# Performance work log

Measured on AMD Instinct MI355X. Metric: run time of the kernel, lower is better.

## Reference

```python
import jax, jax.numpy as jnp
import numpy as np

L = 3          # n_relation_encoder_layer
H = 64         # hidden_dim
PH = 3         # path_hop
SLOPE = (1.0/8.0 + 1.0/3.0) / 2.0  # RReLU in eval mode


def act(x):
    return jnp.where(x >= 0, x, x * SLOPE)


def layer_norm(x, eps=1e-5):
    m = jnp.mean(x, axis=-1, keepdims=True)
    v = jnp.var(x, axis=-1, keepdims=True)
    return (x - m) / jnp.sqrt(v + eps)


def setup_inputs() -> dict:
    key = jax.random.key(0)
    ks = jax.random.split(key, 20)
    E, N, R, Bq = 262144, 65536, 200, 40
    Rt = R * Bq
    d = {}
    d["edge_index"] = jax.random.randint(ks[0], (2, E), 0, N)
    d["edge_type"] = jax.random.randint(ks[1], (E,), 0, Rt)
    d["edge_query_relations"] = jax.random.randint(ks[2], (E,), 0, Rt)
    d["h_positions"] = jax.random.randint(ks[3], (Bq,), 0, N)
    d["t_positions"] = jax.random.randint(ks[4], (Bq,), 0, N)
    d["query_relations"] = jax.random.randint(ks[5], (Bq,), 0, R)
    d["labels"] = jax.random.randint(ks[6], (N, 2), 0, PH + 1)
    d["num_ent"] = N
    d["relation_num"] = R
    d["shot"] = 5
    s = 0.05
    nrm = lambda k, sh: jax.random.normal(k, sh, jnp.float32) * s
    d["pos_emb"] = nrm(ks[7], ((PH + 1) * (PH + 1), H))
    d["start_rel_emb"] = nrm(ks[8], (1, H))
    d["loop_emb"] = nrm(ks[9], (1, H))
    d["W_msg"] = nrm(ks[10], (L, H, 3 * H)); d["b_msg"] = jnp.zeros((L, H))
    d["W_ht2r"] = nrm(ks[11], (L, H, 3 * H)); d["b_ht2r"] = jnp.zeros((L, H))
    d["W_alpha"] = nrm(ks[12], (L, 2 * H)); d["b_alpha"] = jnp.zeros((L,))
    d["W_beta"] = nrm(ks[13], (L, 2 * H)); d["b_beta"] = jnp.zeros((L,))
    d["W_loop"] = nrm(ks[14], (L, H, 2 * H)); d["b_loop"] = jnp.zeros((L, H))
    d["W_ent"] = nrm(ks[15], (L, H, H)); d["b_ent"] = jnp.zeros((L, H))
    d["W_rel"] = nrm(ks[16], (L, H, H)); d["b_rel"] = jnp.zeros((L, H))
    d["W_final"] = nrm(ks[17], (H, L * H)); d["b_final"] = jnp.zeros((H,))
    return d


def reference(pos_emb, start_rel_emb, loop_emb,
              W_msg, b_msg, W_ht2r, b_ht2r, W_alpha, b_alpha, W_beta, b_beta,
              W_loop, b_loop, W_ent, b_ent, W_rel, b_rel, W_final, b_final,
              edge_index, edge_type, edge_query_relations,
              h_positions, t_positions, query_relations, labels,
              num_ent, relation_num, shot):
    Bq = h_positions.shape[0]
    Rt = relation_num * Bq
    col, row = edge_index[0], edge_index[1]  # (h side, t side)

    # token-set initialization
    position = labels[:, 0] * (PH + 1) + labels[:, 1]
    node_emb = pos_emb[position]
    node_emb = node_emb.at[h_positions].set(pos_emb[0])
    node_emb = node_emb.at[t_positions].set(pos_emb[1])
    q_rows = query_relations + jnp.arange(Bq) * relation_num
    rel_emb = jnp.zeros((Rt, H), pos_emb.dtype).at[q_rows].set(start_rel_emb[0])
    loop = jnp.broadcast_to(loop_emb, (Bq, H))

    # compute_norm: symmetric D^-1/2 norm over (col,row)
    deg = jax.ops.segment_sum(jnp.ones((col.shape[0],), node_emb.dtype), row, num_segments=num_ent)
    deg_inv = jnp.where(deg > 0, deg ** -0.5, 0.0)
    ent_norm = deg_inv[row] * deg_inv[col]  # [E]

    finals = []
    for i in range(L):
        r_e = rel_emb[edge_type]            # [E,H]
        h_e = node_emb[col]                 # [E,H]
        q_e = rel_emb[edge_query_relations] # [E,H]
        feat = jnp.concatenate([h_e, r_e, q_e], axis=-1)  # [E,3H]
        msg = act(feat @ W_msg[i].T + b_msg[i])
        # entity attention (GAT); faithful double index_select of the normalizer
        a = act(jnp.concatenate([r_e, q_e], -1)) @ W_alpha[i] + b_alpha[i]  # [E]
        a = jnp.exp(a)
        a_sum = jax.ops.segment_sum(a, row, num_segments=num_ent)
        denom = (a_sum[row] + 1e-10)[row]
        msg = msg * (a / denom)[:, None]
        msg = msg * ent_norm[:, None]   # applied in forward
        msg = msg * ent_norm[:, None]   # applied again in ent_aggregation
        node_emb = jax.ops.segment_sum(msg, row, num_segments=num_ent)
        node_emb = layer_norm(act(node_emb @ W_ent[i].T + b_ent[i]))

        h_e = node_emb[col]
        t_e = node_emb[row]
        r_e = rel_emb[edge_type]
        msg = act(jnp.concatenate([h_e, t_e, q_e], -1) @ W_ht2r[i].T + b_ht2r[i])
        b = jnp.concatenate([r_e, q_e], -1) @ W_beta[i] + b_beta[i]  # no act (as in source)
        b = jnp.exp(b)
        b_sum = jax.ops.segment_sum(b, edge_type, num_segments=Rt)
        b_den = (b_sum[edge_type] + 1e-10)[edge_type]
        msg = msg * (b / b_den)[:, None]
        agg = jax.ops.segment_sum(msg, edge_type, num_segments=Rt)
        rel_emb = layer_norm(act(agg @ W_rel[i].T + b_rel[i]) + rel_emb)
        finals.append(rel_emb)

        qr = rel_emb[q_rows]
        loop = layer_norm(loop + act(jnp.concatenate([loop, qr], -1) @ W_loop[i].T + b_loop[i]))

    fin = jnp.concatenate(finals, axis=-1)            # [Rt, L*H]
    fin = layer_norm(act(fin @ W_final.T + b_final))  # [Rt, H]
    fin = fin.reshape(-1, shot, relation_num, H)
    fin = jnp.mean(fin, axis=1)                       # [B, R, H]; dropout = identity (eval)
    loop_m = jnp.mean(loop.reshape(-1, shot, 1, H), axis=1).reshape(-1, 1, H)
    out = jnp.concatenate([fin, loop_m], axis=1)      # [B, R+1, H]
    return out
```

## Files before the change

kernel.cpp:

```cpp
#include <hip/hip_runtime.h>
#include <hip/hip_bf16.h>

#define DEV __device__ __forceinline__

constexpr int Nn   = 65536;
constexpr int Ee   = 262144;
constexpr int Rr   = 200;
constexpr int BQ   = 40;
constexpr int Rt   = Rr * BQ;
constexpr int Hh   = 64;
constexpr int SHOT = 5;
constexpr float SLOPE  = 0.22916667f;
constexpr float EPS_LN = 1e-5f;

constexpr size_t BASE = 16;
constexpr size_t off_node   = BASE;
constexpr size_t off_node2  = off_node  + (size_t)Nn*32;
constexpr size_t off_rel    = off_node2 + (size_t)Nn*32;
constexpr size_t off_rel2   = off_rel   + (size_t)Rt*32;
constexpr size_t off_fin    = off_rel2  + (size_t)Rt*32;
constexpr size_t off_finln  = off_fin   + (size_t)3*Rt*32;
constexpr size_t off_loop   = off_finln + (size_t)Rt*Hh;
constexpr size_t off_avP    = off_loop  + (size_t)BQ*Hh;
constexpr size_t off_bvP    = off_avP   + (size_t)Ee;
constexpr size_t off_asum   = off_bvP   + (size_t)Ee;
constexpr size_t off_bsum   = off_asum  + (size_t)Nn;
constexpr size_t off_degF   = off_bsum  + (size_t)Rt;
constexpr size_t off_degi   = off_degF  + (size_t)Nn;
constexpr size_t off_histE  = off_degi  + (size_t)Nn;
constexpr size_t off_baseE  = off_histE + (size_t)Rt;
constexpr size_t off_baseR  = off_baseE + (size_t)Rt;
constexpr size_t off_part   = off_baseR + (size_t)Nn;
constexpr size_t off_uv     = off_part  + 256;
constexpr size_t off_edge1  = off_uv    + (size_t)4*Rt;
constexpr size_t off_edge2  = off_edge1 + (size_t)4*Ee;
constexpr size_t off_WmsgF  = off_edge2 + (size_t)4*Ee;
constexpr size_t off_Wht2rF = off_WmsgF + 18432;
constexpr size_t off_WentF  = off_Wht2rF + 18432;
constexpr size_t off_WrelF  = off_WentF + 6144;
constexpr size_t off_WfinF  = off_WrelF + 6144;
constexpr size_t off_Wloop  = off_WfinF + 6144;
constexpr size_t off_bmsg   = off_Wloop + (size_t)3*128*64;
constexpr size_t off_bht2r  = off_bmsg  + 192;
constexpr size_t off_bent   = off_bht2r + 192;
constexpr size_t off_brel   = off_bent  + 192;
constexpr size_t off_bloop  = off_brel  + 192;
constexpr size_t off_bfin   = off_bloop + 192;
constexpr size_t off_Wa     = off_bfin  + 64;
constexpr size_t off_ba     = off_Wa    + 384;
constexpr size_t off_Wb     = off_ba    + 4;
constexpr size_t off_bb     = off_Wb    + 384;
constexpr size_t off_pos    = off_bb    + 4;
constexpr size_t off_srel   = off_pos   + 1024;
constexpr size_t off_loop0  = off_srel  + 64;
constexpr size_t off_end    = off_loop0 + 64;

typedef __attribute__((ext_vector_type(8))) short short8v;
typedef __attribute__((ext_vector_type(4))) float float4v;

DEV float bf2f(unsigned short u) { return __uint_as_float(((unsigned)u) << 16); }
DEV unsigned short f2bf_rtne(float f) {
    unsigned int b = __float_as_uint(f);
    b += 0x7FFFu + ((b >> 16) & 1u);
    return (unsigned short)(b >> 16);
}
DEV float actf(float x) { return x >= 0.f ? x : x * SLOPE; }
DEV void atomAddF(float* p, float v) {
#if defined(__HIP_DEVICE_COMPILE__)
    unsafeAtomicAdd(p, v);
#endif
}
DEV void atomPkAddBf16(unsigned short* p, unsigned int pk) {
#if defined(__HIP_DEVICE_COMPILE__)
    asm volatile("global_atomic_pk_add_bf16 %0, %1, off"
                 :: "v"((unsigned long long)p), "v"(pk) : "memory");
#endif
}
DEV float loadF(const void* p, size_t i, int isb) {
    return isb ? bf2f(((const unsigned short*)p)[i]) : ((const float*)p)[i];
}

__global__ __launch_bounds__(64) void k_sniff(const unsigned short* __restrict__ pos, int* __restrict__ flag) {
    float v = bf2f(pos[threadIdx.x]);
    bool bad = !(fabsf(v) < 1e3f);
    unsigned long long m = __ballot(bad);
    if (threadIdx.x == 0) flag[0] = (m == 0ull) ? 1 : 0;
}

__global__ __launch_bounds__(256) void k_fill16(unsigned short* __restrict__ out, int n, unsigned short val) {
    int i = blockIdx.x * 256 + threadIdx.x;
    if (i < n) out[i] = val;
}

struct PrepArgs { const void* src[19]; void* dst[19]; };

__global__ __launch_bounds__(256) void k_prep(PrepArgs a, const int* __restrict__ flag,
                                              int* __restrict__ degi, unsigned int* __restrict__ relz,
                                              int* __restrict__ histE) {
    constexpr int NJ = 19;
    constexpr int type[NJ] = {3,3,3,3,3,2, 0,0,0,0,0,0,0,0,0,0,0,0,0};
    constexpr int KD[NJ]   = {192,192,64,64,192,128, 0,0,0,0,0,0,0,0,0,0,0,0,0};
    constexpr int NEL[NJ]  = {36864,36864,12288,12288,12288,24576,
                              192,192,192,192,192,64,384,3,384,3,1024,64,64};
    const int isb = flag[0];
    int tid0 = blockIdx.x * blockDim.x + threadIdx.x;
    int stride = gridDim.x * blockDim.x;
    for (int j = 0; j < NJ; ++j) {
        const void* s = a.src[j];
        int n = NEL[j];
        if (type[j] == 0) {
            float* d = (float*)a.dst[j];
            for (int i = tid0; i < n; i += stride) d[i] = loadF(s, i, isb);
        } else if (type[j] == 2) {
            float* d = (float*)a.dst[j];
            int K = KD[j];
            for (int i = tid0; i < n; i += stride) {
                int h = i & 63;
                int k = (i >> 6) % K;
                int b = i / (64 * K);
                d[i] = loadF(s, (size_t)(b*64 + h) * K + k, isb);
            }
        } else {
            unsigned short* d = (unsigned short*)a.dst[j];
            int K = KD[j];
            int perL = K * 64;
            for (int i = tid0; i < n; i += stride) {
                int layer = i / perL;
                int r1 = i % perL;
                int c  = r1 / 2048;
                int r2 = r1 % 2048;
                int g  = r2 / 512;
                int r3 = r2 % 512;
                int l  = r3 >> 3;
                int jj = r3 & 7;
                int nn = g * 16 + (l & 15);
                int k  = c * 32 + (l >> 4) * 8 + jj;
                d[i] = f2bf_rtne(loadF(s, (size_t)layer * perL + (size_t)nn * K + k, isb));
            }
        }
    }
    for (int i = tid0; i < Nn; i += stride) degi[i] = 0;
    for (int i = tid0; i < Rt * 32; i += stride) relz[i] = 0u;
    for (int i = tid0; i < Rt; i += stride) histE[i] = 0;
}

__global__ __launch_bounds__(256) void k_hist(const int* __restrict__ rowp, const int* __restrict__ et,
                                              int* __restrict__ degi, int* __restrict__ histE) {
    int e = blockIdx.x * 256 + threadIdx.x;
    if (e < Ee) {
        atomicAdd(&degi[rowp[e]], 1);
        atomicAdd(&histE[et[e]], 1);
    }
}

__global__ __launch_bounds__(256) void k_deg_scan(const int* __restrict__ degi, float* __restrict__ degF,
                                                  int* __restrict__ part,
                                                  const int* __restrict__ histE, int* __restrict__ baseE) {
    __shared__ int sh[256];
    __shared__ int sh2[256];
    int t = threadIdx.x, b = blockIdx.x;
    int n = b * 256 + t;
    int d = degi[n];
    degF[n] = d > 0 ? 1.0f / sqrtf((float)d) : 0.0f;
    sh[t] = d; __syncthreads();
    for (int o = 128; o; o >>= 1) { if (t < o) sh[t] += sh[t + o]; __syncthreads(); }
    if (t == 0) part[b] = sh[0];
    if (b == 0) {
        int s = 0;
        for (int j = 0; j < 32; ++j) { int idx = t * 32 + j; if (idx < Rt) s += histE[idx]; }
        sh2[t] = s; __syncthreads();
        for (int o = 1; o < 256; o <<= 1) {
            int u = (t >= o) ? sh2[t - o] : 0;
            __syncthreads(); sh2[t] += u; __syncthreads();
        }
        int run = sh2[t] - s;
        for (int j = 0; j < 32; ++j) {
            int idx = t * 32 + j;
            if (idx < Rt) { baseE[idx] = run; run += histE[idx]; }
        }
    }
}

__global__ __launch_bounds__(256) void k_scan_part(int* __restrict__ part) {
    __shared__ int sh[256];
    int t = threadIdx.x;
    int v = part[t];
    sh[t] = v; __syncthreads();
    for (int o = 1; o < 256; o <<= 1) {
        int u = (t >= o) ? sh[t - o] : 0;
        __syncthreads(); sh[t] += u; __syncthreads();
    }
    part[t] = sh[t] - v;
}

__global__ __launch_bounds__(256) void k_baseR(const int* __restrict__ degi, const int* __restrict__ part,
                                               int* __restrict__ baseR) {
    __shared__ int sh[256];
    int t = threadIdx.x, b = blockIdx.x;
    int n = b * 256 + t;
    int d = degi[n];
    sh[t] = d; __syncthreads();
    for (int o = 1; o < 256; o <<= 1) {
        int u = (t >= o) ? sh[t - o] : 0;
        __syncthreads(); sh[t] += u; __syncthreads();
    }
    baseR[n] = part[b] + sh[t] - d;
}

__global__ __launch_bounds__(256) void k_scatter(const int* __restrict__ col, const int* __restrict__ rowp,
                                                 const int* __restrict__ et, const int* __restrict__ eqr,
                                                 int* __restrict__ baseR, int* __restrict__ baseE,
                                                 int4* __restrict__ edge1, int4* __restrict__ edge2) {
    int e = blockIdx.x * 256 + threadIdx.x;
    if (e >= Ee) return;
    int4 ed; ed.x = col[e]; ed.y = rowp[e]; ed.z = et[e]; ed.w = eqr[e];
    int s1 = atomicAdd(&baseR[ed.y], 1);
    edge1[s1] = ed;
    int s2 = atomicAdd(&baseE[ed.z], 1);
    edge2[s2] = ed;
}

__global__ __launch_bounds__(256) void k_node_init(const int* __restrict__ labels,
                                                   const float* __restrict__ posf,
                                                   unsigned short* __restrict__ node) {
    int idx = blockIdx.x * 256 + threadIdx.x;
    if (idx >= Nn * Hh) return;
    int n = idx >> 6, h = idx & 63;
    int pos = labels[2*n] * 4 + labels[2*n + 1];
    node[idx] = f2bf_rtne(posf[pos * 64 + h]);
}
__global__ __launch_bounds__(256) void k_init_small(const int* __restrict__ hpos, const int* __restrict__ tpos,
                                                    const int* __restrict__ qrel,
                                                    const float* __restrict__ posf,
                                                    const float* __restrict__ srel,
                                                    const float* __restrict__ l0,
                                                    unsigned short* __restrict__ node,
                                                    unsigned short* __restrict__ rel,
                                                    float* __restrict__ loop) {
    int idx = blockIdx.x * 256 + threadIdx.x;
    int seg = idx / (BQ * Hh), r = idx % (BQ * Hh);
    int b = r >> 6, h = r & 63;
    if (seg == 0) {
        int p = hpos[b];
        bool skip = false;
        for (int j = 0; j < BQ; ++j) skip |= (tpos[j] == p);
        if (!skip) node[(size_t)p * 64 + h] = f2bf_rtne(posf[h]);
    } else if (seg == 1) {
        node[(size_t)tpos[b] * 64 + h] = f2bf_rtne(posf[64 + h]);
    } else if (seg == 2) {
        rel[((size_t)qrel[b] + (size_t)b * Rr) * 64 + h] = f2bf_rtne(srel[h]);
    } else if (seg == 3) {
        loop[r] = l0[h];
    }
}

__global__ __launch_bounds__(256) void k_uv(const unsigned short* __restrict__ rel,
                                            const float* __restrict__ Wa, const float* __restrict__ Wb,
                                            float* __restrict__ uv,
                                            float* __restrict__ asum,
                                            float4v* __restrict__ node2, float4v* __restrict__ rel2) {
    int tid = threadIdx.x, lane = tid & 63, wv = tid >> 6;
    int w = blockIdx.x * 4 + wv;
    if (w < Rt) {
        float x = bf2f(rel[(size_t)w * 64 + lane]);
        float ax = actf(x);
        float pua = ax * Wa[lane], pva = ax * Wa[64 + lane];
        float pub = x * Wb[lane],  pvb = x * Wb[64 + lane];
        for (int off = 32; off; off >>= 1) {
            pua += __shfl_xor(pua, off); pva += __shfl_xor(pva, off);
            pub += __shfl_xor(pub, off); pvb += __shfl_xor(pvb, off);
        }
        if (lane == 0) {
            uv[w] = pua; uv[Rt + w] = pva; uv[2 * Rt + w] = pub; uv[3 * Rt + w] = pvb;
        }
    }
    int tid0 = blockIdx.x * 256 + tid;
    int stride = gridDim.x * 256;
    float4v z = {0.f, 0.f, 0.f, 0.f};
    for (int i = tid0; i < Nn + Rt; i += stride) asum[i] = 0.f;
    for (int i = tid0; i < Nn * 8; i += stride) node2[i] = z;
    for (int i = tid0; i < Rt * 8; i += stride) rel2[i] = z;
}

__global__ __launch_bounds__(256) void k_ab_edge(const int4* __restrict__ edge1, const int4* __restrict__ edge2,
                                                 const float* __restrict__ uv,
                                                 const float* __restrict__ ba, const float* __restrict__ bb,
                                                 float* __restrict__ avP, float* __restrict__ bvP,
                                                 float* __restrict__ a_sum, float* __restrict__ b_sum) {
    __shared__ float sv[256];
    __shared__ int sd[256];
    int tid = threadIdx.x;
    int e = blockIdx.x * 256 + tid;
    int4 e1 = edge1[e];
    float av = expf(uv[e1.z] + uv[Rt + e1.w] + ba[0]);
    avP[e] = av;
    sv[tid] = av; sd[tid] = e1.y;
    __syncthreads();
    if (tid == 0 || sd[tid - 1] != e1.y) {
        float s = av;
        for (int j = tid + 1; j < 256 && sd[j] == e1.y; ++j) s += sv[j];
        atomAddF(&a_sum[e1.y], s);
    }
    __syncthreads();
    int4 e2 = edge2[e];
    float bv = expf(uv[2 * Rt + e2.z] + uv[3 * Rt + e2.w] + bb[0]);
    bvP[e] = bv;
    sv[tid] = bv; sd[tid] = e2.z;
    __syncthreads();
    if (tid == 0 || sd[tid - 1] != e2.z) {
        float s = bv;
        for (int j = tid + 1; j < 256 && sd[j] == e2.z; ++j) s += sv[j];
        atomAddF(&b_sum[e2.z], s);
    }
}

template<int KIND>
__global__ __launch_bounds__(256) void k_msg_mfma(
    const unsigned short* __restrict__ node, const unsigned short* __restrict__ rel,
    const int4* __restrict__ edgeP,
    const int* __restrict__ rowp_orig, const int* __restrict__ et_orig,
    const unsigned short* __restrict__ Wfrag,
    const float* __restrict__ bias,
    const float* __restrict__ vals, const float* __restrict__ sums,
    const float* __restrict__ degF,
    unsigned short* __restrict__ dst)
{
    constexpr int P = 200;
    __shared__ __align__(16) unsigned short feat[64 * P];
    __shared__ int s_src0[64], s_src1[64], s_src2[64], s_dst[64];
    __shared__ float s_coeff[64];
    const int tid = threadIdx.x;
    const int lane = tid & 63;
    const int wv = tid >> 6;
    const int e0 = blockIdx.x * 64;

    if (tid < 64) {
        int e = e0 + tid;
        int4 ed = edgeP[e];
        if (KIND == 0) {
            s_src0[tid] = ed.x; s_src1[tid] = ed.z; s_src2[tid] = ed.w; s_dst[tid] = ed.y;
            int rr = rowp_orig[ed.y];
            float dn = degF[ed.y] * degF[ed.x];
            s_coeff[tid] = vals[e] / (sums[rr] + 1e-10f) * dn * dn;
        } else {
            s_src0[tid] = ed.x; s_src1[tid] = ed.y; s_src2[tid] = ed.w; s_dst[tid] = ed.z;
            int tt = et_orig[ed.z];
            s_coeff[tid] = vals[e] / (sums[tt] + 1e-10f);
        }
    }

    const int wr = wv >> 1, wc = wv & 1;
    short8v bf[2][6];
#pragma unroll
    for (int tc = 0; tc < 2; ++tc) {
        int g = wc * 2 + tc;
#pragma unroll
        for (int c = 0; c < 6; ++c)
            bf[tc][c] = *(const short8v*)(Wfrag + (((size_t)c * 4 + g) * 64 + lane) * 8);
    }
    __syncthreads();

    {
        const int sub = lane >> 3, ls8 = lane & 7;
#pragma unroll
        for (int t2 = 0; t2 < 6; ++t2) {
            int unit = wv * 48 + t2 * 8 + sub;
            int e = unit & 63, part = unit >> 6;
            int srow = part == 0 ? s_src0[e] : (part == 1 ? s_src1[e] : s_src2[e]);
            const unsigned short* bse;
            if (KIND == 0) bse = (part == 0) ? node : rel;
            else           bse = (part == 2) ? rel : node;
            uint4 v = *(const uint4*)(bse + (size_t)srow * 64 + ls8 * 8);
            *(uint4*)(feat + (size_t)e * P + part * 64 + ls8 * 8) = v;
        }
    }
    __syncthreads();

    const int m = lane & 15, qd = lane >> 4;
    float4v zero = {0.f, 0.f, 0.f, 0.f};
    float4v acc[2][2];
    acc[0][0] = zero; acc[0][1] = zero; acc[1][0] = zero; acc[1][1] = zero;
#pragma unroll
    for (int c = 0; c < 6; ++c) {
        short8v a0 = *(const short8v*)(feat + (wr * 32 + m) * P + c * 32 + qd * 8);
        short8v a1 = *(const short8v*)(feat + (wr * 32 + 16 + m) * P + c * 32 + qd * 8);
        acc[0][0] = __builtin_amdgcn_mfma_f32_16x16x32_bf16(a0, bf[0][c], acc[0][0], 0, 0, 0);
        acc[0][1] = __builtin_amdgcn_mfma_f32_16x16x32_bf16(a0, bf[1][c], acc[0][1], 0, 0, 0);
        acc[1][0] = __builtin_amdgcn_mfma_f32_16x16x32_bf16(a1, bf[0][c], acc[1][0], 0, 0, 0);
        acc[1][1] = __builtin_amdgcn_mfma_f32_16x16x32_bf16(a1, bf[1][c], acc[1][1], 0, 0, 0);
    }
    __syncthreads();

    float* msgT = (float*)feat;
#pragma unroll
    for (int tc = 0; tc < 2; ++tc) {
        int h = wc * 32 + tc * 16 + m;
        float bi = bias[h];
#pragma unroll
        for (int tr = 0; tr < 2; ++tr) {
#pragma unroll
            for (int r = 0; r < 4; ++r) {
                int er = wr * 32 + tr * 16 + qd * 4 + r;
                msgT[er * 65 + h] = actf(acc[tr][tc][r] + bi) * s_coeff[er];
            }
        }
    }
    __syncthreads();

    {
        int c = wv * 16 + (lane & 15);
        int seg = lane >> 4;
        int ebase = seg * 16;
        float a = 0.f;
#pragma unroll
        for (int i = 0; i < 16; ++i) {
            int e = ebase + i;
            a += msgT[e * 65 + c];
            bool flush = (i == 15) || (s_dst[e + 1] != s_dst[e]);
            float an = __shfl_xor(a, 1);
            if (flush) {
                if (!(lane & 1)) {
                    unsigned int pk = (unsigned int)f2bf_rtne(a)
                                    | ((unsigned int)f2bf_rtne(an) << 16);
                    atomPkAddBf16(dst + (size_t)s_dst[e] * 64 + c, pk);
                }
                a = 0.f;
            }
        }
    }
#if defined(__HIP_DEVICE_COMPILE__)
    asm volatile("s_waitcnt vmcnt(0)" ::: "memory");
#endif
}

template<int MODE>
__global__ __launch_bounds__(256) void k_row_ln(const unsigned short* __restrict__ x,
                                                const unsigned short* __restrict__ Wfrag,
                                                const float* __restrict__ bias,
                                                unsigned short* __restrict__ out,
                                                unsigned short* __restrict__ fin_i) {
    __shared__ float yT[64 * 65];
    const int tid = threadIdx.x, lane = tid & 63, wv = tid >> 6;
    const int wr = wv >> 1, wc = wv & 1;
    const int m = lane & 15, qd = lane >> 4;
    const size_t n0 = (size_t)blockIdx.x * 64;

    short8v bf[2][2];
#pragma unroll
    for (int tc = 0; tc < 2; ++tc) {
        int g = wc * 2 + tc;
#pragma unroll
        for (int c = 0; c < 2; ++c)
            bf[tc][c] = *(const short8v*)(Wfrag + (((size_t)c * 4 + g) * 64 + lane) * 8);
    }

    float4v zero = {0.f, 0.f, 0.f, 0.f};
    float4v acc[2][2];
    acc[0][0] = zero; acc[0][1] = zero; acc[1][0] = zero; acc[1][1] = zero;
#pragma unroll
    for (int c = 0; c < 2; ++c) {
        short8v a0 = *(const short8v*)(x + (n0 + wr * 32 + m) * 64 + c * 32 + qd * 8);
        short8v a1 = *(const short8v*)(x + (n0 + wr * 32 + 16 + m) * 64 + c * 32 + qd * 8);
        acc[0][0] = __builtin_amdgcn_mfma_f32_16x16x32_bf16(a0, bf[0][c], acc[0][0], 0, 0, 0);
        acc[0][1] = __builtin_amdgcn_mfma_f32_16x16x32_bf16(a0, bf[1][c], acc[0][1], 0, 0, 0);
        acc[1][0] = __builtin_amdgcn_mfma_f32_16x16x32_bf16(a1, bf[0][c], acc[1][0], 0, 0, 0);
        acc[1][1] = __builtin_amdgcn_mfma_f32_16x16x32_bf16(a1, bf[1][c], acc[1][1], 0, 0, 0);
    }

#pragma unroll
    for (int tc = 0; tc < 2; ++tc) {
        int h = wc * 32 + tc * 16 + m;
        float bi = bias[h];
#pragma unroll
        for (int tr = 0; tr < 2; ++tr) {
#pragma unroll
            for (int r = 0; r < 4; ++r) {
                int row = wr * 32 + tr * 16 + qd * 4 + r;
                yT[row * 65 + h] = actf(acc[tr][tc][r] + bi);
            }
        }
    }
    __syncthreads();

    for (int jj = 0; jj < 16; ++jj) {
        int j = wv * 16 + jj;
        float v = yT[j * 65 + lane];
        if (MODE == 1) v += bf2f(out[(n0 + j) * 64 + lane]);
        float s = v, s2 = v * v;
        for (int off = 32; off; off >>= 1) { s += __shfl_xor(s, off); s2 += __shfl_xor(s2, off); }
        float mean = s * (1.f / 64.f);
        float var = s2 * (1.f / 64.f) - mean * mean;
        if (var < 0.f) var = 0.f;
        unsigned short nv = f2bf_rtne((v - mean) / sqrtf(var + EPS_LN));
        out[(n0 + j) * 64 + lane] = nv;
        if (MODE == 1) fin_i[(n0 + j) * 64 + lane] = nv;
    }
}

__global__ __launch_bounds__(256) void k_final(const unsigned short* __restrict__ finB,
                                               const unsigned short* __restrict__ Wfrag,
                                               const float* __restrict__ bias,
                                               float* __restrict__ fin_ln) {
    __shared__ float yT[64 * 65];
    const int tid = threadIdx.x, lane = tid & 63, wv = tid >> 6;
    const int wr = wv >> 1, wc = wv & 1;
    const int m = lane & 15, qd = lane >> 4;
    const size_t r0 = (size_t)blockIdx.x * 64;

    short8v bf[2][6];
#pragma unroll
    for (int tc = 0; tc < 2; ++tc) {
        int g = wc * 2 + tc;
#pragma unroll
        for (int c = 0; c < 6; ++c)
            bf[tc][c] = *(const short8v*)(Wfrag + (((size_t)c * 4 + g) * 64 + lane) * 8);
    }

    float4v zero = {0.f, 0.f, 0.f, 0.f};
    float4v acc[2][2];
    acc[0][0] = zero; acc[0][1] = zero; acc[1][0] = zero; acc[1][1] = zero;
#pragma unroll
    for (int c = 0; c < 6; ++c) {
        const unsigned short* base = finB + (size_t)(c >> 1) * Rt * 64 + (c & 1) * 32 + qd * 8;
        short8v a0 = *(const short8v*)(base + (r0 + wr * 32 + m) * 64);
        short8v a1 = *(const short8v*)(base + (r0 + wr * 32 + 16 + m) * 64);
        acc[0][0] = __builtin_amdgcn_mfma_f32_16x16x32_bf16(a0, bf[0][c], acc[0][0], 0, 0, 0);
        acc[0][1] = __builtin_amdgcn_mfma_f32_16x16x32_bf16(a0, bf[1][c], acc[0][1], 0, 0, 0);
        acc[1][0] = __builtin_amdgcn_mfma_f32_16x16x32_bf16(a1, bf[0][c], acc[1][0], 0, 0, 0);
        acc[1][1] = __builtin_amdgcn_mfma_f32_16x16x32_bf16(a1, bf[1][c], acc[1][1], 0, 0, 0);
    }

#pragma unroll
    for (int tc = 0; tc < 2; ++tc) {
        int h = wc * 32 + tc * 16 + m;
        float bi = bias[h];
#pragma unroll
        for (int tr = 0; tr < 2; ++tr) {
#pragma unroll
            for (int r = 0; r < 4; ++r) {
                int row = wr * 32 + tr * 16 + qd * 4 + r;
                yT[row * 65 + h] = actf(acc[tr][tc][r] + bi);
            }
        }
    }
    __syncthreads();

    for (int jj = 0; jj < 16; ++jj) {
        int j = wv * 16 + jj;
        float v = yT[j * 65 + lane];
        float s = v, s2 = v * v;
        for (int off = 32; off; off >>= 1) { s += __shfl_xor(s, off); s2 += __shfl_xor(s2, off); }
        float mean = s * (1.f / 64.f);
        float var = s2 * (1.f / 64.f) - mean * mean;
        if (var < 0.f) var = 0.f;
        fin_ln[(r0 + j) * 64 + lane] = (v - mean) / sqrtf(var + EPS_LN);
    }
}

__global__ __launch_bounds__(64) void k_loop_upd(const unsigned short* __restrict__ rel,
                                                 const int* __restrict__ qrel,
                                                 const float* __restrict__ Wt,
                                                 const float* __restrict__ bias,
                                                 float* __restrict__ loop) {
    __shared__ float cat[128];
    int b = blockIdx.x, lane = threadIdx.x;
    float lv = loop[b * 64 + lane];
    int qr = qrel[b] + b * Rr;
    cat[lane] = lv;
    cat[64 + lane] = bf2f(rel[(size_t)qr * 64 + lane]);
    __syncthreads();
    float acc = 0.f;
    for (int k = 0; k < 128; ++k) acc = fmaf(cat[k], Wt[k * 64 + lane], acc);
    float v = lv + actf(acc + bias[lane]);
    float s = v, s2 = v * v;
    for (int off = 32; off; off >>= 1) { s += __shfl_xor(s, off); s2 += __shfl_xor(s2, off); }
    float mean = s * (1.f / 64.f);
    float var = s2 * (1.f / 64.f) - mean * mean;
    if (var < 0.f) var = 0.f;
    loop[b * 64 + lane] = (v - mean) / sqrtf(var + EPS_LN);
}

__global__ __launch_bounds__(256) void k_out(const float* __restrict__ fin_ln,
                                             const float* __restrict__ loop,
                                             void* __restrict__ out, int n,
                                             const int* __restrict__ flag) {
    int idx = blockIdx.x * 256 + threadIdx.x;
    if (idx >= n) return;
    int h = idx & 63;
    int j = (idx >> 6) % (Rr + 1);
    int g = idx / ((Rr + 1) * 64);
    float v = 0.f;
    if (j < Rr) {
        for (int s = 0; s < SHOT; ++s)
            v += fin_ln[(size_t)((g * SHOT + s) * Rr + j) * 64 + h];
    } else {
        for (int s = 0; s < SHOT; ++s)
            v += loop[(g * SHOT + s) * 64 + h];
    }
    v *= (1.0f / SHOT);
    if (flag[0]) ((__hip_bfloat16*)out)[idx] = __float2bfloat16(v);
    else         ((float*)out)[idx] = v;
}

extern "C" void kernel_launch(void* const* d_in, const int* in_sizes, int n_in,
                              void* d_out, int out_size, void* d_ws, size_t ws_size,
                              hipStream_t stream) {
    if (ws_size < off_end * 4 || n_in != 29) {
        k_fill16<<<(out_size + 255) / 256, 256, 0, stream>>>(
            (unsigned short*)d_out, out_size, (n_in != 29) ? (unsigned short)0x429A : (unsigned short)0x42F6);
        return;
    }

    const int* edge_index = (const int*)d_in[0];
    const int* col  = edge_index;
    const int* rowp = edge_index + Ee;
    const int* et   = (const int*)d_in[1];
    const int* eqr  = (const int*)d_in[2];
    const int* hpos = (const int*)d_in[3];
    const int* tpos = (const int*)d_in[4];
    const int* qrel = (const int*)d_in[5];
    const int* labels = (const int*)d_in[6];

    float* W = (float*)d_ws;
    int*   flag  = (int*)d_ws;
    unsigned short* node  = (unsigned short*)(W + off_node);
    unsigned short* node2 = (unsigned short*)(W + off_node2);
    unsigned short* rel   = (unsigned short*)(W + off_rel);
    unsigned short* rel2  = (unsigned short*)(W + off_rel2);
    unsigned short* fin   = (unsigned short*)(W + off_fin);
    float* finln = W + off_finln;
    float* loop  = W + off_loop;
    float* avP   = W + off_avP;
    float* bvP   = W + off_bvP;
    float* asum  = W + off_asum;
    float* bsum  = W + off_bsum;
    float* degF  = W + off_degF;
    int*   degi  = (int*)(W + off_degi);
    int*   histE = (int*)(W + off_histE);
    int*   baseE = (int*)(W + off_baseE);
    int*   baseR = (int*)(W + off_baseR);
    int*   part  = (int*)(W + off_part);
    float* uv    = W + off_uv;
    int4*  edge1 = (int4*)(W + off_edge1);
    int4*  edge2 = (int4*)(W + off_edge2);
    unsigned short* WmsgF  = (unsigned short*)(W + off_WmsgF);
    unsigned short* Wht2rF = (unsigned short*)(W + off_Wht2rF);
    unsigned short* WentF  = (unsigned short*)(W + off_WentF);
    unsigned short* WrelF  = (unsigned short*)(W + off_WrelF);
    unsigned short* WfinF  = (unsigned short*)(W + off_WfinF);

    k_sniff<<<1, 64, 0, stream>>>((const unsigned short*)d_in[10], flag);
    PrepArgs pa;
    const int src_idx[19] = {13,15,23,25,27,21, 14,16,24,26,22,28,17,18,19,20,10,11,12};
    void* dsts[19] = {WmsgF, Wht2rF, WentF, WrelF, WfinF, W+off_Wloop,
                      W+off_bmsg, W+off_bht2r, W+off_bent, W+off_brel, W+off_bloop, W+off_bfin,
                      W+off_Wa, W+off_ba, W+off_Wb, W+off_bb, W+off_pos, W+off_srel, W+off_loop0};
    for (int j = 0; j < 19; ++j) { pa.src[j] = d_in[src_idx[j]]; pa.dst[j] = dsts[j]; }
    k_prep<<<144, 256, 0, stream>>>(pa, flag, degi, (unsigned int*)rel, histE);

    k_hist<<<Ee / 256, 256, 0, stream>>>(rowp, et, degi, histE);
    k_deg_scan<<<Nn / 256, 256, 0, stream>>>(degi, degF, part, histE, baseE);
    k_scan_part<<<1, 256, 0, stream>>>(part);
    k_baseR<<<Nn / 256, 256, 0, stream>>>(degi, part, baseR);
    k_scatter<<<Ee / 256, 256, 0, stream>>>(col, rowp, et, eqr, baseR, baseE, edge1, edge2);
    k_node_init<<<(Nn * Hh) / 256, 256, 0, stream>>>(labels, W + off_pos, node);
    k_init_small<<<(4 * BQ * Hh + 255) / 256, 256, 0, stream>>>(hpos, tpos, qrel,
                                                                W + off_pos, W + off_srel, W + off_loop0,
                                                                node, rel, loop);

    for (int i = 0; i < 3; ++i) {
        k_uv<<<2048, 256, 0, stream>>>(rel, W + off_Wa + i * 128, W + off_Wb + i * 128,
                                       uv, asum, (float4v*)node2, (float4v*)rel2);
        k_ab_edge<<<Ee / 256, 256, 0, stream>>>(edge1, edge2, uv,
                                                W + off_ba + i, W + off_bb + i,
                                                avP, bvP, asum, bsum);
        k_msg_mfma<0><<<Ee / 64, 256, 0, stream>>>(node, rel, edge1, rowp, et,
                                                   WmsgF + (size_t)i * 12288, W + off_bmsg + i * 64,
                                                   avP, asum, degF, node2);
        k_row_ln<0><<<Nn / 64, 256, 0, stream>>>(node2, WentF + (size_t)i * 4096,
                                                 W + off_bent + i * 64, node, nullptr);
        k_msg_mfma<1><<<Ee / 64, 256, 0, stream>>>(node, rel, edge2, rowp, et,
                                                   Wht2rF + (size_t)i * 12288, W + off_bht2r + i * 64,
                                                   bvP, bsum, degF, rel2);
        k_row_ln<1><<<Rt / 64, 256, 0, stream>>>(rel2, WrelF + (size_t)i * 4096,
                                                 W + off_brel + i * 64, rel,
                                                 fin + (size_t)i * Rt * 64);
        k_loop_upd<<<BQ, 64, 0, stream>>>(rel, qrel, W + off_Wloop + (size_t)i * 8192,
                                          W + off_bloop + i * 64, loop);
    }

    k_final<<<Rt / 64, 256, 0, stream>>>(fin, WfinF, W + off_bfin, finln);
    k_out<<<(out_size + 255) / 256, 256, 0, stream>>>(finln, loop, d_out, out_size, flag);
}
```

Before: 567.1 us.

## Fuse uv/zeroing/loop update into LN kernels and double edges per msg block

Removes the per-layer k_uv and k_loop_upd kernels. Their work moves into other kernels: the uv projection for the next layer is computed inside the new k_rel_ln, the loop update runs there too, and the accumulator zeroing is done inside the LN kernels right after they read their inputs. Node init and the first-layer uv are folded into k_prep and k_init_small. Separately, k_msg_mfma now handles 128 edges per block in two 64-edge passes, halving the grid and reusing the weight fragments held in registers. The aim is fewer launches and less global traffic, at the cost of more serial work per block and careful ordering of the zeroing against later reads.

New measurement: 606.5 us. +6.9%, slower.

```diff
diff --git a/kernel.cpp b/kernel.cpp
--- a/kernel.cpp
+++ b/kernel.cpp
@@ -96,7 +96,12 @@
 
 __global__ __launch_bounds__(256) void k_prep(PrepArgs a, const int* __restrict__ flag,
                                               int* __restrict__ degi, unsigned int* __restrict__ relz,
-                                              int* __restrict__ histE) {
+                                              int* __restrict__ histE,
+                                              const int* __restrict__ labels, const void* __restrict__ pos_raw,
+                                              unsigned short* __restrict__ node,
+                                              unsigned int* __restrict__ node2z, unsigned int* __restrict__ rel2z,
+                                              float* __restrict__ asumz,
+                                              float* __restrict__ uvz) {
     constexpr int NJ = 19;
     constexpr int type[NJ] = {3,3,3,3,3,2, 0,0,0,0,0,0,0,0,0,0,0,0,0};
     constexpr int KD[NJ]   = {192,192,64,64,192,128, 0,0,0,0,0,0,0,0,0,0,0,0,0};
@@ -139,9 +144,18 @@
             }
         }
     }
+    for (int i = tid0; i < Nn * Hh; i += stride) {
+        int n = i >> 6, h = i & 63;
+        int pos = labels[2*n] * 4 + labels[2*n + 1];
+        node[i] = f2bf_rtne(loadF(pos_raw, (size_t)pos * 64 + h, isb));
+    }
     for (int i = tid0; i < Nn; i += stride) degi[i] = 0;
     for (int i = tid0; i < Rt * 32; i += stride) relz[i] = 0u;
     for (int i = tid0; i < Rt; i += stride) histE[i] = 0;
+    for (int i = tid0; i < Nn * 32; i += stride) node2z[i] = 0u;
+    for (int i = tid0; i < Rt * 32; i += stride) rel2z[i] = 0u;
+    for (int i = tid0; i < Nn + Rt; i += stride) asumz[i] = 0.f;
+    for (int i = tid0; i < 4 * Rt; i += stride) uvz[i] = 0.f;
 }
 
 __global__ __launch_bounds__(256) void k_hist(const int* __restrict__ rowp, const int* __restrict__ et,
@@ -220,15 +234,6 @@
     edge2[s2] = ed;
 }
 
-__global__ __launch_bounds__(256) void k_node_init(const int* __restrict__ labels,
-                                                   const float* __restrict__ posf,
-                                                   unsigned short* __restrict__ node) {
-    int idx = blockIdx.x * 256 + threadIdx.x;
-    if (idx >= Nn * Hh) return;
-    int n = idx >> 6, h = idx & 63;
-    int pos = labels[2*n] * 4 + labels[2*n + 1];
-    node[idx] = f2bf_rtne(posf[pos * 64 + h]);
-}
 __global__ __launch_bounds__(256) void k_init_small(const int* __restrict__ hpos, const int* __restrict__ tpos,
                                                     const int* __restrict__ qrel,
                                                     const float* __restrict__ posf,
@@ -236,7 +241,9 @@
                                                     const float* __restrict__ l0,
                                                     unsigned short* __restrict__ node,
                                                     unsigned short* __restrict__ rel,
-                                                    float* __restrict__ loop) {
+                                                    float* __restrict__ loop,
+                                                    const float* __restrict__ Wa0, const float* __restrict__ Wb0,
+                                                    float* __restrict__ uv) {
     int idx = blockIdx.x * 256 + threadIdx.x;
     int seg = idx / (BQ * Hh), r = idx % (BQ * Hh);
     int b = r >> 6, h = r & 63;
@@ -248,38 +255,23 @@
     } else if (seg == 1) {
         node[(size_t)tpos[b] * 64 + h] = f2bf_rtne(posf[64 + h]);
     } else if (seg == 2) {
-        rel[((size_t)qrel[b] + (size_t)b * Rr) * 64 + h] = f2bf_rtne(srel[h]);
-    } else if (seg == 3) {
-        loop[r] = l0[h];
-    }
-}
-
-__global__ __launch_bounds__(256) void k_uv(const unsigned short* __restrict__ rel,
-                                            const float* __restrict__ Wa, const float* __restrict__ Wb,
-                                            float* __restrict__ uv,
-                                            float* __restrict__ asum,
-                                            float4v* __restrict__ node2, float4v* __restrict__ rel2) {
-    int tid = threadIdx.x, lane = tid & 63, wv = tid >> 6;
-    int w = blockIdx.x * 4 + wv;
-    if (w < Rt) {
-        float x = bf2f(rel[(size_t)w * 64 + lane]);
+        int w = qrel[b] + b * Rr;
+        unsigned short xb = f2bf_rtne(srel[h]);
+        rel[(size_t)w * 64 + h] = xb;
+        float x = bf2f(xb);
         float ax = actf(x);
-        float pua = ax * Wa[lane], pva = ax * Wa[64 + lane];
-        float pub = x * Wb[lane],  pvb = x * Wb[64 + lane];
+        float pua = ax * Wa0[h], pva = ax * Wa0[64 + h];
+        float pub = x * Wb0[h],  pvb = x * Wb0[64 + h];
         for (int off = 32; off; off >>= 1) {
             pua += __shfl_xor(pua, off); pva += __shfl_xor(pva, off);
             pub += __shfl_xor(pub, off); pvb += __shfl_xor(pvb, off);
         }
-        if (lane == 0) {
+        if (h == 0) {
             uv[w] = pua; uv[Rt + w] = pva; uv[2 * Rt + w] = pub; uv[3 * Rt + w] = pvb;
         }
-    }
-    int tid0 = blockIdx.x * 256 + tid;
-    int stride = gridDim.x * 256;
-    float4v z = {0.f, 0.f, 0.f, 0.f};
-    for (int i = tid0; i < Nn + Rt; i += stride) asum[i] = 0.f;
-    for (int i = tid0; i < Nn * 8; i += stride) node2[i] = z;
-    for (int i = tid0; i < Rt * 8; i += stride) rel2[i] = z;
+    } else if (seg == 3) {
+        loop[r] = l0[h];
+    }
 }
 
 __global__ __launch_bounds__(256) void k_ab_edge(const int4* __restrict__ edge1, const int4* __restrict__ edge2,
@@ -327,14 +319,14 @@
 {
     constexpr int P = 200;
     __shared__ __align__(16) unsigned short feat[64 * P];
-    __shared__ int s_src0[64], s_src1[64], s_src2[64], s_dst[64];
-    __shared__ float s_coeff[64];
+    __shared__ int s_src0[128], s_src1[128], s_src2[128], s_dst[132];
+    __shared__ float s_coeff[128];
     const int tid = threadIdx.x;
     const int lane = tid & 63;
     const int wv = tid >> 6;
-    const int e0 = blockIdx.x * 64;
-
-    if (tid < 64) {
+    const int e0 = blockIdx.x * 128;
+
+    if (tid < 128) {
         int e = e0 + tid;
         int4 ed = edgeP[e];
         if (KIND == 0) {
@@ -348,6 +340,7 @@
             s_coeff[tid] = vals[e] / (sums[tt] + 1e-10f);
         }
     }
+    if (tid == 0) s_dst[128] = -1;
 
     const int wr = wv >> 1, wc = wv & 1;
     short8v bf[2][6];
@@ -360,85 +353,88 @@
     }
     __syncthreads();
 
-    {
-        const int sub = lane >> 3, ls8 = lane & 7;
+    const int sub = lane >> 3, ls8 = lane & 7;
+    const int m = lane & 15, qd = lane >> 4;
+
+#pragma unroll 1
+    for (int t = 0; t < 2; ++t) {
+        const int tb = t * 64;
 #pragma unroll
         for (int t2 = 0; t2 < 6; ++t2) {
             int unit = wv * 48 + t2 * 8 + sub;
             int e = unit & 63, part = unit >> 6;
-            int srow = part == 0 ? s_src0[e] : (part == 1 ? s_src1[e] : s_src2[e]);
+            int srow = part == 0 ? s_src0[tb + e] : (part == 1 ? s_src1[tb + e] : s_src2[tb + e]);
             const unsigned short* bse;
             if (KIND == 0) bse = (part == 0) ? node : rel;
             else           bse = (part == 2) ? rel : node;
             uint4 v = *(const uint4*)(bse + (size_t)srow * 64 + ls8 * 8);
             *(uint4*)(feat + (size_t)e * P + part * 64 + ls8 * 8) = v;
         }
-    }
-    __syncthreads();
-
-    const int m = lane & 15, qd = lane >> 4;
-    float4v zero = {0.f, 0.f, 0.f, 0.f};
-    float4v acc[2][2];
-    acc[0][0] = zero; acc[0][1] = zero; acc[1][0] = zero; acc[1][1] = zero;
-#pragma unroll
-    for (int c = 0; c < 6; ++c) {
-        short8v a0 = *(const short8v*)(feat + (wr * 32 + m) * P + c * 32 + qd * 8);
-        short8v a1 = *(const short8v*)(feat + (wr * 32 + 16 + m) * P + c * 32 + qd * 8);
-        acc[0][0] = __builtin_amdgcn_mfma_f32_16x16x32_bf16(a0, bf[0][c], acc[0][0], 0, 0, 0);
-        acc[0][1] = __builtin_amdgcn_mfma_f32_16x16x32_bf16(a0, bf[1][c], acc[0][1], 0, 0, 0);
-        acc[1][0] = __builtin_amdgcn_mfma_f32_16x16x32_bf16(a1, bf[0][c], acc[1][0], 0, 0, 0);
-        acc[1][1] = __builtin_amdgcn_mfma_f32_16x16x32_bf16(a1, bf[1][c], acc[1][1], 0, 0, 0);
-    }
-    __syncthreads();
-
-    float* msgT = (float*)feat;
-#pragma unroll
-    for (int tc = 0; tc < 2; ++tc) {
-        int h = wc * 32 + tc * 16 + m;
-        float bi = bias[h];
-#pragma unroll
-        for (int tr = 0; tr < 2; ++tr) {
-#pragma unroll
-            for (int r = 0; r < 4; ++r) {
-                int er = wr * 32 + tr * 16 + qd * 4 + r;
-                msgT[er * 65 + h] = actf(acc[tr][tc][r] + bi) * s_coeff[er];
-            }
-        }
-    }
-    __syncthreads();
-
-    {
-        int c = wv * 16 + (lane & 15);
-        int seg = lane >> 4;
-        int ebase = seg * 16;
-        float a = 0.f;
-#pragma unroll
-        for (int i = 0; i < 16; ++i) {
-            int e = ebase + i;
-            a += msgT[e * 65 + c];
-            bool flush = (i == 15) || (s_dst[e + 1] != s_dst[e]);
-            float an = __shfl_xor(a, 1);
-            if (flush) {
-                if (!(lane & 1)) {
-                    unsigned int pk = (unsigned int)f2bf_rtne(a)
-                                    | ((unsigned int)f2bf_rtne(an) << 16);
-                    atomPkAddBf16(dst + (size_t)s_dst[e] * 64 + c, pk);
+        __syncthreads();
+
+        float4v zero = {0.f, 0.f, 0.f, 0.f};
+        float4v acc[2][2];
+        acc[0][0] = zero; acc[0][1] = zero; acc[1][0] = zero; acc[1][1] = zero;
+#pragma unroll
+        for (int c = 0; c < 6; ++c) {
+            short8v a0 = *(const short8v*)(feat + (wr * 32 + m) * P + c * 32 + qd * 8);
+            short8v a1 = *(const short8v*)(feat + (wr * 32 + 16 + m) * P + c * 32 + qd * 8);
+            acc[0][0] = __builtin_amdgcn_mfma_f32_16x16x32_bf16(a0, bf[0][c], acc[0][0], 0, 0, 0);
+            acc[0][1] = __builtin_amdgcn_mfma_f32_16x16x32_bf16(a0, bf[1][c], acc[0][1], 0, 0, 0);
+            acc[1][0] = __builtin_amdgcn_mfma_f32_16x16x32_bf16(a1, bf[0][c], acc[1][0], 0, 0, 0);
+            acc[1][1] = __builtin_amdgcn_mfma_f32_16x16x32_bf16(a1, bf[1][c], acc[1][1], 0, 0, 0);
+        }
+        __syncthreads();
+
+        float* msgT = (float*)feat;
+#pragma unroll
+        for (int tc = 0; tc < 2; ++tc) {
+            int h = wc * 32 + tc * 16 + m;
+            float bi = bias[h];
+#pragma unroll
+            for (int tr = 0; tr < 2; ++tr) {
+#pragma unroll
+                for (int r = 0; r < 4; ++r) {
+                    int er = wr * 32 + tr * 16 + qd * 4 + r;
+                    msgT[er * 65 + h] = actf(acc[tr][tc][r] + bi) * s_coeff[tb + er];
                 }
-                a = 0.f;
-            }
-        }
+            }
+        }
+        __syncthreads();
+
+        {
+            int c = wv * 16 + (lane & 15);
+            int seg = lane >> 4;
+            int ebase = seg * 16;
+            float a = 0.f;
+#pragma unroll
+            for (int i = 0; i < 16; ++i) {
+                int el = ebase + i;
+                a += msgT[el * 65 + c];
+                bool flush = (i == 15) || (s_dst[tb + el + 1] != s_dst[tb + el]);
+                float an = __shfl_xor(a, 1);
+                if (flush) {
+                    if (!(lane & 1)) {
+                        unsigned int pk = (unsigned int)f2bf_rtne(a)
+                                        | ((unsigned int)f2bf_rtne(an) << 16);
+                        atomPkAddBf16(dst + (size_t)s_dst[tb + el] * 64 + c, pk);
+                    }
+                    a = 0.f;
+                }
+            }
+        }
+        __syncthreads();
     }
 #if defined(__HIP_DEVICE_COMPILE__)
     asm volatile("s_waitcnt vmcnt(0)" ::: "memory");
 #endif
 }
 
-template<int MODE>
-__global__ __launch_bounds__(256) void k_row_ln(const unsigned short* __restrict__ x,
+__global__ __launch_bounds__(256) void k_ent_ln(unsigned short* __restrict__ x,
                                                 const unsigned short* __restrict__ Wfrag,
                                                 const float* __restrict__ bias,
                                                 unsigned short* __restrict__ out,
-                                                unsigned short* __restrict__ fin_i) {
+                                                float* __restrict__ asum) {
     __shared__ float yT[64 * 65];
     const int tid = threadIdx.x, lane = tid & 63, wv = tid >> 6;
     const int wr = wv >> 1, wc = wv & 1;
@@ -482,18 +478,132 @@
     }
     __syncthreads();
 
+    {
+        unsigned int* xz = (unsigned int*)(x + n0 * 64);
+#pragma unroll
+        for (int i = 0; i < 8; ++i) xz[tid + i * 256] = 0u;
+        if (tid < 64) asum[blockIdx.x * 64 + tid] = 0.f;
+    }
+
     for (int jj = 0; jj < 16; ++jj) {
         int j = wv * 16 + jj;
         float v = yT[j * 65 + lane];
-        if (MODE == 1) v += bf2f(out[(n0 + j) * 64 + lane]);
         float s = v, s2 = v * v;
         for (int off = 32; off; off >>= 1) { s += __shfl_xor(s, off); s2 += __shfl_xor(s2, off); }
         float mean = s * (1.f / 64.f);
         float var = s2 * (1.f / 64.f) - mean * mean;
         if (var < 0.f) var = 0.f;
-        unsigned short nv = f2bf_rtne((v - mean) / sqrtf(var + EPS_LN));
-        out[(n0 + j) * 64 + lane] = nv;
-        if (MODE == 1) fin_i[(n0 + j) * 64 + lane] = nv;
+        out[(n0 + j) * 64 + lane] = f2bf_rtne((v - mean) / sqrtf(var + EPS_LN));
+    }
+}
+
+__global__ __launch_bounds__(256) void k_rel_ln(unsigned short* __restrict__ x,
+                                                const unsigned short* __restrict__ Wfrag,
+                                                const float* __restrict__ bias,
+                                                unsigned short* __restrict__ rel,
+                                                unsigned short* __restrict__ fin_i,
+                                                float* __restrict__ bsum,
+                                                const float* __restrict__ WaN, const float* __restrict__ WbN,
+                                                float* __restrict__ uvN,
+                                                const int* __restrict__ qrel,
+                                                const float* __restrict__ Wt,
+                                                const float* __restrict__ bloop,
+                                                float* __restrict__ loop) {
+    __shared__ float yT[64 * 65];
+    const int tid = threadIdx.x, lane = tid & 63, wv = tid >> 6;
+    const int wr = wv >> 1, wc = wv & 1;
+    const int m = lane & 15, qd = lane >> 4;
+    const size_t r0 = (size_t)blockIdx.x * 64;
+
+    short8v bf[2][2];
+#pragma unroll
+    for (int tc = 0; tc < 2; ++tc) {
+        int g = wc * 2 + tc;
+#pragma unroll
+        for (int c = 0; c < 2; ++c)
+            bf[tc][c] = *(const short8v*)(Wfrag + (((size_t)c * 4 + g) * 64 + lane) * 8);
+    }
+
+    float4v zero = {0.f, 0.f, 0.f, 0.f};
+    float4v acc[2][2];
+    acc[0][0] = zero; acc[0][1] = zero; acc[1][0] = zero; acc[1][1] = zero;
+#pragma unroll
+    for (int c = 0; c < 2; ++c) {
+        short8v a0 = *(const short8v*)(x + (r0 + wr * 32 + m) * 64 + c * 32 + qd * 8);
+        short8v a1 = *(const short8v*)(x + (r0 + wr * 32 + 16 + m) * 64 + c * 32 + qd * 8);
+        acc[0][0] = __builtin_amdgcn_mfma_f32_16x16x32_bf16(a0, bf[0][c], acc[0][0], 0, 0, 0);
+        acc[0][1] = __builtin_amdgcn_mfma_f32_16x16x32_bf16(a0, bf[1][c], acc[0][1], 0, 0, 0);
+        acc[1][0] = __builtin_amdgcn_mfma_f32_16x16x32_bf16(a1, bf[0][c], acc[1][0], 0, 0, 0);
+        acc[1][1] = __builtin_amdgcn_mfma_f32_16x16x32_bf16(a1, bf[1][c], acc[1][1], 0, 0, 0);
+    }
+
+#pragma unroll
+    for (int tc = 0; tc < 2; ++tc) {
+        int h = wc * 32 + tc * 16 + m;
+        float bi = bias[h];
+#pragma unroll
+        for (int tr = 0; tr < 2; ++tr) {
+#pragma unroll
+            for (int r = 0; r < 4; ++r) {
+                int row = wr * 32 + tr * 16 + qd * 4 + r;
+                yT[row * 65 + h] = actf(acc[tr][tc][r] + bi);
+            }
+        }
+    }
+    __syncthreads();
+
+    {
+        unsigned int* xz = (unsigned int*)(x + r0 * 64);
+#pragma unroll
+        for (int i = 0; i < 8; ++i) xz[tid + i * 256] = 0u;
+        if (tid < 64) bsum[blockIdx.x * 64 + tid] = 0.f;
+    }
+
+    for (int jj = 0; jj < 16; ++jj) {
+        int j = wv * 16 + jj;
+        float v = yT[j * 65 + lane] + bf2f(rel[(r0 + j) * 64 + lane]);
+        float s = v, s2 = v * v;
+        for (int off = 32; off; off >>= 1) { s += __shfl_xor(s, off); s2 += __shfl_xor(s2, off); }
+        float mean = s * (1.f / 64.f);
+        float var = s2 * (1.f / 64.f) - mean * mean;
+        if (var < 0.f) var = 0.f;
+        float nv = (v - mean) / sqrtf(var + EPS_LN);
+        unsigned short nb = f2bf_rtne(nv);
+        rel[(r0 + j) * 64 + lane] = nb;
+        fin_i[(r0 + j) * 64 + lane] = nb;
+        yT[j * 65 + lane] = nv;
+        if (uvN) {
+            float ax = actf(nv);
+            float pua = ax * WaN[lane], pva = ax * WaN[64 + lane];
+            float pub = nv * WbN[lane], pvb = nv * WbN[64 + lane];
+            for (int off = 32; off; off >>= 1) {
+                pua += __shfl_xor(pua, off); pva += __shfl_xor(pva, off);
+                pub += __shfl_xor(pub, off); pvb += __shfl_xor(pvb, off);
+            }
+            if (lane == 0) {
+                size_t w = r0 + j;
+                uvN[w] = pua; uvN[Rt + w] = pva; uvN[2 * Rt + w] = pub; uvN[3 * Rt + w] = pvb;
+            }
+        }
+    }
+    __syncthreads();
+
+    if (wv == 0) {
+        for (int b = 0; b < BQ; ++b) {
+            int loc = qrel[b] + b * Rr - (int)r0;
+            if (loc < 0 || loc >= 64) continue;
+            float lv = loop[b * 64 + lane];
+            float acc2 = 0.f;
+            for (int k = 0; k < 64; ++k) acc2 = fmaf(__shfl(lv, k), Wt[k * 64 + lane], acc2);
+            for (int k = 0; k < 64; ++k) acc2 = fmaf(yT[loc * 65 + k], Wt[(64 + k) * 64 + lane], acc2);
+            float v = lv + actf(acc2 + bloop[lane]);
+            float s = v, s2 = v * v;
+            for (int off = 32; off; off >>= 1) { s += __shfl_xor(s, off); s2 += __shfl_xor(s2, off); }
+            float mean = s * (1.f / 64.f);
+            float var = s2 * (1.f / 64.f) - mean * mean;
+            if (var < 0.f) var = 0.f;
+            loop[b * 64 + lane] = (v - mean) / sqrtf(var + EPS_LN);
+        }
     }
 }
 
@@ -555,29 +665,6 @@
         if (var < 0.f) var = 0.f;
         fin_ln[(r0 + j) * 64 + lane] = (v - mean) / sqrtf(var + EPS_LN);
     }
-}
-
-__global__ __launch_bounds__(64) void k_loop_upd(const unsigned short* __restrict__ rel,
-                                                 const int* __restrict__ qrel,
-                                                 const float* __restrict__ Wt,
-                                                 const float* __restrict__ bias,
-                                                 float* __restrict__ loop) {
-    __shared__ float cat[128];
-    int b = blockIdx.x, lane = threadIdx.x;
-    float lv = loop[b * 64 + lane];
-    int qr = qrel[b] + b * Rr;
-    cat[lane] = lv;
-    cat[64 + lane] = bf2f(rel[(size_t)qr * 64 + lane]);
-    __syncthreads();
-    float acc = 0.f;
-    for (int k = 0; k < 128; ++k) acc = fmaf(cat[k], Wt[k * 64 + lane], acc);
-    float v = lv + actf(acc + bias[lane]);
-    float s = v, s2 = v * v;
-    for (int off = 32; off; off >>= 1) { s += __shfl_xor(s, off); s2 += __shfl_xor(s2, off); }
-    float mean = s * (1.f / 64.f);
-    float var = s2 * (1.f / 64.f) - mean * mean;
-    if (var < 0.f) var = 0.f;
-    loop[b * 64 + lane] = (v - mean) / sqrtf(var + EPS_LN);
 }
 
 __global__ __launch_bounds__(256) void k_out(const float* __restrict__ fin_ln,
@@ -656,37 +743,40 @@
                       W+off_bmsg, W+off_bht2r, W+off_bent, W+off_brel, W+off_bloop, W+off_bfin,
                       W+off_Wa, W+off_ba, W+off_Wb, W+off_bb, W+off_pos, W+off_srel, W+off_loop0};
     for (int j = 0; j < 19; ++j) { pa.src[j] = d_in[src_idx[j]]; pa.dst[j] = dsts[j]; }
-    k_prep<<<144, 256, 0, stream>>>(pa, flag, degi, (unsigned int*)rel, histE);
+    k_prep<<<512, 256, 0, stream>>>(pa, flag, degi, (unsigned int*)rel, histE,
+                                    labels, d_in[10], node,
+                                    (unsigned int*)node2, (unsigned int*)rel2, asum, uv);
 
     k_hist<<<Ee / 256, 256, 0, stream>>>(rowp, et, degi, histE);
     k_deg_scan<<<Nn / 256, 256, 0, stream>>>(degi, degF, part, histE, baseE);
     k_scan_part<<<1, 256, 0, stream>>>(part);
     k_baseR<<<Nn / 256, 256, 0, stream>>>(degi, part, baseR);
     k_scatter<<<Ee / 256, 256, 0, stream>>>(col, rowp, et, eqr, baseR, baseE, edge1, edge2);
-    k_node_init<<<(Nn * Hh) / 256, 256, 0, stream>>>(labels, W + off_pos, node);
     k_init_small<<<(4 * BQ * Hh + 255) / 256, 256, 0, stream>>>(hpos, tpos, qrel,
                                                                 W + off_pos, W + off_srel, W + off_loop0,
-                                                                node, rel, loop);
+                                                                node, rel, loop,
+                                                                W + off_Wa, W + off_Wb, uv);
 
     for (int i = 0; i < 3; ++i) {
-        k_uv<<<2048, 256, 0, stream>>>(rel, W + off_Wa + i * 128, W + off_Wb + i * 128,
-                                       uv, asum, (float4v*)node2, (float4v*)rel2);
         k_ab_edge<<<Ee / 256, 256, 0, stream>>>(edge1, edge2, uv,
                                                 W + off_ba + i, W + off_bb + i,
                                                 avP, bvP, asum, bsum);
-        k_msg_mfma<0><<<Ee / 64, 256, 0, stream>>>(node, rel, edge1, rowp, et,
-                                                   WmsgF + (size_t)i * 12288, W + off_bmsg + i * 64,
-                                                   avP, asum, degF, node2);
-        k_row_ln<0><<<Nn / 64, 256, 0, stream>>>(node2, WentF + (size_t)i * 4096,
-                                                 W + off_bent + i * 64, node, nullptr);
-        k_msg_mfma<1><<<Ee / 64, 256, 0, stream>>>(node, rel, edge2, rowp, et,
-                                                   Wht2rF + (size_t)i * 12288, W + off_bht2r + i * 64,
-                                                   bvP, bsum, degF, rel2);
-        k_row_ln<1><<<Rt / 64, 256, 0, stream>>>(rel2, WrelF + (size_t)i * 4096,
-                                                 W + off_brel + i * 64, rel,
-                                                 fin + (size_t)i * Rt * 64);
-        k_loop_upd<<<BQ, 64, 0, stream>>>(rel, qrel, W + off_Wloop + (size_t)i * 8192,
-                                          W + off_bloop + i * 64, loop);
+        k_msg_mfma<0><<<Ee / 128, 256, 0, stream>>>(node, rel, edge1, rowp, et,
+                                                    WmsgF + (size_t)i * 12288, W + off_bmsg + i * 64,
+                                                    avP, asum, degF, node2);
+        k_ent_ln<<<Nn / 64, 256, 0, stream>>>(node2, WentF + (size_t)i * 4096,
+                                              W + off_bent + i * 64, node, asum);
+        k_msg_mfma<1><<<Ee / 128, 256, 0, stream>>>(node, rel, edge2, rowp, et,
+                                                    Wht2rF + (size_t)i * 12288, W + off_bht2r + i * 64,
+                                                    bvP, bsum, degF, rel2);
+        const float* WaN = (i < 2) ? W + off_Wa + (i + 1) * 128 : nullptr;
+        const float* WbN = (i < 2) ? W + off_Wb + (i + 1) * 128 : nullptr;
+        k_rel_ln<<<Rt / 64, 256, 0, stream>>>(rel2, WrelF + (size_t)i * 4096,
+                                              W + off_brel + i * 64, rel,
+                                              fin + (size_t)i * Rt * 64,
+                                              bsum, WaN, WbN, (i < 2) ? uv : nullptr,
+                                              qrel, W + off_Wloop + (size_t)i * 8192,
+                                              W + off_bloop + i * 64, loop);
     }
 
     k_final<<<Rt / 64, 256, 0, stream>>>(fin, WfinF, W + off_bfin, finln);
```
